# Optimization experiments

Hardware: AMD Instinct MI355X
Metric: run time of the kernel (lower is better)

The kernel has to match this reference:

```python
import jax, jax.numpy as jnp
import numpy as np

NUM_HEADS = 8
DIM = 64
DEPTH = DIM // NUM_HEADS  # 8
F = 64  # input feature dim


def setup_inputs() -> dict:
    key = jax.random.key(0)
    ks = jax.random.split(key, 5)
    x = jax.random.normal(ks[0], (4, 2048, F), dtype=jnp.float32)
    # per-head weights stacked: [H, F, depth]; initializer 'normal' ~ N(0, 0.05) in keras,
    # but scale does not change the math structure; use small normal.
    Wq = jax.random.normal(ks[1], (NUM_HEADS, F, DEPTH), dtype=jnp.float32) * 0.05
    Wk = jax.random.normal(ks[2], (NUM_HEADS, F, DEPTH), dtype=jnp.float32) * 0.05
    Wv = jax.random.normal(ks[3], (NUM_HEADS, F, DEPTH), dtype=jnp.float32) * 0.05
    Wo = jax.random.normal(ks[4], (NUM_HEADS * DEPTH, F), dtype=jnp.float32) * 0.05
    return {"x": x, "Wq": Wq, "Wk": Wk, "Wv": Wv, "Wo": Wo}


def reference(x, Wq, Wk, Wv, Wo):
    # x: [B, S, F]; Wq/Wk/Wv: [H, F, D]; Wo: [H*D, F]
    q = jnp.einsum("bsf,hfd->hbsd", x, Wq)
    k = jnp.einsum("bsf,hfd->hbsd", x, Wk)
    v = jnp.einsum("bsf,hfd->hbsd", x, Wv)
    scores = jnp.einsum("hbsd,hbtd->hbst", q, k) / jnp.sqrt(jnp.float32(DEPTH))
    weights = jax.nn.softmax(scores, axis=-1)  # [H, B, S, S]
    heads = jnp.einsum("hbst,hbtd->hbsd", weights, v)  # [H, B, S, D]
    # concat heads along last dim -> [B, S, H*D]
    B, S = x.shape[0], x.shape[1]
    concat = jnp.transpose(heads, (1, 2, 0, 3)).reshape(B, S, NUM_HEADS * DEPTH)
    out = concat @ Wo  # [B, S, F]
    # return_sequences=False -> sum over sequence axis
    return jnp.sum(out, axis=1), weights
```

## Files before the change

### kernel.cpp

```cpp
#include <hip/hip_runtime.h>
#include <cstdint>
#include <cstddef>

#define NH 8
#define NB 4
#define SS 2048
#define FF 64
#define DD 8
#define QKV_SZ (NH*NB*SS*DD)

typedef float f32x2 __attribute__((ext_vector_type(2)));

__device__ __forceinline__ f32x2 pkfma(f32x2 a, f32x2 b, f32x2 c) {
#if __has_builtin(__builtin_elementwise_fma)
  return __builtin_elementwise_fma(a, b, c);
#else
  f32x2 r; r.x = fmaf(a.x, b.x, c.x); r.y = fmaf(a.y, b.y, c.y); return r;
#endif
}

__device__ __forceinline__ float fastexp2(float x) {
#if __has_builtin(__builtin_amdgcn_exp2f)
  return __builtin_amdgcn_exp2f(x);
#else
  return exp2f(x);
#endif
}

__device__ __forceinline__ f32x2 lo2(float4 v) { f32x2 r; r.x = v.x; r.y = v.y; return r; }
__device__ __forceinline__ f32x2 hi2(float4 v) { f32x2 r; r.x = v.z; r.y = v.w; return r; }

__device__ __forceinline__ float wave_sum64(float x) {
#define DPP_STEP(ctrl, rm) { int t_ = __builtin_amdgcn_update_dpp(0, __float_as_int(x), (ctrl), (rm), 0xf, true); x += __int_as_float(t_); }
  DPP_STEP(0x111, 0xf)
  DPP_STEP(0x112, 0xf)
  DPP_STEP(0x114, 0xf)
  DPP_STEP(0x118, 0xf)
  DPP_STEP(0x142, 0xa)
  DPP_STEP(0x143, 0xc)
#undef DPP_STEP
  return x;
}

__global__ __launch_bounds__(256) void qkv_kernel(
    const float* __restrict__ x,
    const float* __restrict__ Wq, const float* __restrict__ Wk, const float* __restrict__ Wv,
    float* __restrict__ Qo, float* __restrict__ Ko, float* __restrict__ Vo) {
  __shared__ float xT[64][65];
  const int tid = threadIdx.x;
  const int row0 = blockIdx.x * 64;
  #pragma unroll
  for (int k = 0; k < 4; ++k) {
    int flat4 = tid + 256 * k;
    int r = flat4 >> 4, fq = flat4 & 15;
    float4 xv = reinterpret_cast<const float4*>(x)[(size_t)(row0 + r) * 16 + fq];
    xT[fq * 4 + 0][r] = xv.x; xT[fq * 4 + 1][r] = xv.y;
    xT[fq * 4 + 2][r] = xv.z; xT[fq * 4 + 3][r] = xv.w;
  }
  __syncthreads();
  const int r = tid & 63;
  const int wg = __builtin_amdgcn_readfirstlane((int)(blockIdx.y * 4 + (tid >> 6)));
  const float* Wmh[3];
  #pragma unroll
  for (int j = 0; j < 3; ++j) {
    int c = wg * 3 + j;
    int m = c >> 3, h = c & 7;
    const float* Wsel = (m == 0) ? Wq : ((m == 1) ? Wk : Wv);
    Wmh[j] = Wsel + (h << 9);
  }
  float acc[3][8];
  #pragma unroll
  for (int j = 0; j < 3; ++j)
    #pragma unroll
    for (int d = 0; d < 8; ++d) acc[j][d] = 0.f;
  for (int f = 0; f < 64; ++f) {
    float xv = xT[f][r];
    #pragma unroll
    for (int j = 0; j < 3; ++j) {
      const float4* wp = reinterpret_cast<const float4*>(Wmh[j] + f * 8);
      float4 wa = wp[0], wb = wp[1];
      acc[j][0] = fmaf(xv, wa.x, acc[j][0]); acc[j][1] = fmaf(xv, wa.y, acc[j][1]);
      acc[j][2] = fmaf(xv, wa.z, acc[j][2]); acc[j][3] = fmaf(xv, wa.w, acc[j][3]);
      acc[j][4] = fmaf(xv, wb.x, acc[j][4]); acc[j][5] = fmaf(xv, wb.y, acc[j][5]);
      acc[j][6] = fmaf(xv, wb.z, acc[j][6]); acc[j][7] = fmaf(xv, wb.w, acc[j][7]);
    }
  }
  const int row = row0 + r;
  const int b = row >> 11, s = row & 2047;
  const float qscale = 0.35355339059327373f * 1.4426950408889634f;
  #pragma unroll
  for (int j = 0; j < 3; ++j) {
    int c = wg * 3 + j;
    int m = c >> 3, h = c & 7;
    float sc = (m == 0) ? qscale : 1.f;
    float* dst = ((m == 0) ? Qo : ((m == 1) ? Ko : Vo)) + (((size_t)(h * NB + b) * SS) + s) * DD;
    float4 o0 = make_float4(acc[j][0] * sc, acc[j][1] * sc, acc[j][2] * sc, acc[j][3] * sc);
    float4 o1 = make_float4(acc[j][4] * sc, acc[j][5] * sc, acc[j][6] * sc, acc[j][7] * sc);
    reinterpret_cast<float4*>(dst)[0] = o0;
    reinterpret_cast<float4*>(dst)[1] = o1;
  }
}

__global__ __launch_bounds__(256, 4) void attn_kernel(
    const float* __restrict__ Qg, const float* __restrict__ Kg, const float* __restrict__ Vg,
    float* __restrict__ wOut, float* __restrict__ hsum2) {
  __shared__ float4 klds[4 * 512];
  __shared__ float4 qlds[128];
  __shared__ float psum[4][64];
  __shared__ float nls_s[64];
  __shared__ float hred[4][8];
  const int tid = threadIdx.x;
  const int lane = tid & 63;
  const int w = tid >> 6;
  const int bx = blockIdx.x;
  const int hb = bx >> 5;
  const int rt = bx & 31;
  const int r0 = rt * 64;
  const float* Kbase = Kg + (size_t)hb * SS * DD;
  const float* Vbase = Vg + (size_t)hb * SS * DD;
  const float4* K4 = reinterpret_cast<const float4*>(Kbase);
  const float4* Q4 = reinterpret_cast<const float4*>(Qg + (size_t)hb * SS * DD + (size_t)r0 * DD);
  float* wBase = wOut + (size_t)hb * SS * SS + (size_t)r0 * SS;

  if (tid < 128) qlds[tid] = Q4[tid];

  float4 qa = Q4[lane * 2], qb = Q4[lane * 2 + 1];
  f32x2 q01, q23, q45, q67;
  q01.x = qa.x; q01.y = qa.y; q23.x = qa.z; q23.y = qa.w;
  q45.x = qb.x; q45.y = qb.y; q67.x = qb.z; q67.y = qb.w;
  float rs0 = 0.f, rs1 = 0.f;
  float4* kw = klds + w * 512;
  for (int cc = 0; cc < 2; ++cc) {
    const int t0 = (w * 2 + cc) * 256;
    #pragma unroll
    for (int i = 0; i < 8; ++i) kw[lane + 64 * i] = K4[(size_t)t0 * 2 + lane + 64 * i];
    float4 a0 = kw[0], b0 = kw[1], a1 = kw[2], b1 = kw[3];
    float4 a2 = kw[4], b2 = kw[5], a3 = kw[6], b3 = kw[7];
    for (int tt = 0; tt < 256; tt += 4) {
      const int tn = (tt + 4 < 256) ? (tt + 4) : 0;
      float4 na0 = kw[2 * tn],     nb0 = kw[2 * tn + 1];
      float4 na1 = kw[2 * tn + 2], nb1 = kw[2 * tn + 3];
      float4 na2 = kw[2 * tn + 4], nb2 = kw[2 * tn + 5];
      float4 na3 = kw[2 * tn + 6], nb3 = kw[2 * tn + 7];
      f32x2 d0 = q01 * lo2(a0);
      d0 = pkfma(q23, hi2(a0), d0); d0 = pkfma(q45, lo2(b0), d0); d0 = pkfma(q67, hi2(b0), d0);
      f32x2 d1 = q01 * lo2(a1);
      d1 = pkfma(q23, hi2(a1), d1); d1 = pkfma(q45, lo2(b1), d1); d1 = pkfma(q67, hi2(b1), d1);
      f32x2 d2 = q01 * lo2(a2);
      d2 = pkfma(q23, hi2(a2), d2); d2 = pkfma(q45, lo2(b2), d2); d2 = pkfma(q67, hi2(b2), d2);
      f32x2 d3 = q01 * lo2(a3);
      d3 = pkfma(q23, hi2(a3), d3); d3 = pkfma(q45, lo2(b3), d3); d3 = pkfma(q67, hi2(b3), d3);
      rs0 += fastexp2(d0.x + d0.y) + fastexp2(d1.x + d1.y);
      rs1 += fastexp2(d2.x + d2.y) + fastexp2(d3.x + d3.y);
      a0 = na0; b0 = nb0; a1 = na1; b1 = nb1;
      a2 = na2; b2 = nb2; a3 = na3; b3 = nb3;
    }
  }
  psum[w][lane] = rs0 + rs1;
  __syncthreads();
  if (tid < 64)
    nls_s[tid] = -log2f(psum[0][tid] + psum[1][tid] + psum[2][tid] + psum[3][tid]);
  __syncthreads();

  float A[8] = {0.f, 0.f, 0.f, 0.f, 0.f, 0.f, 0.f, 0.f};
  for (int ci = 0; ci < 2; ++ci) {
    const int c = w * 2 + ci;
    const int tbase = c * 256;
    const int tl = tbase + 4 * lane;
    const float4* kp = reinterpret_cast<const float4*>(Kbase + (size_t)tl * DD);
    float4 k0a = kp[0], k0b = kp[1], k1a = kp[2], k1b = kp[3];
    float4 k2a = kp[4], k2b = kp[5], k3a = kp[6], k3b = kp[7];
    float4 qa2 = qlds[0], qb2 = qlds[1];
    float nl = nls_s[0];
    float cs0 = 0.f, cs1 = 0.f, cs2 = 0.f, cs3 = 0.f;
    for (int r = 0; r < 64; ++r) {
      const int rn = (r < 63) ? (r + 1) : 63;
      float4 na = qlds[rn * 2], nb = qlds[rn * 2 + 1];
      float nln = nls_s[rn];
      f32x2 p01, p23, p45, p67, seed;
      p01.x = qa2.x; p01.y = qa2.y; p23.x = qa2.z; p23.y = qa2.w;
      p45.x = qb2.x; p45.y = qb2.y; p67.x = qb2.z; p67.y = qb2.w;
      seed.x = nl; seed.y = 0.f;
      f32x2 d0 = pkfma(p01, lo2(k0a), seed);
      d0 = pkfma(p23, hi2(k0a), d0); d0 = pkfma(p45, lo2(k0b), d0); d0 = pkfma(p67, hi2(k0b), d0);
      f32x2 d1 = pkfma(p01, lo2(k1a), seed);
      d1 = pkfma(p23, hi2(k1a), d1); d1 = pkfma(p45, lo2(k1b), d1); d1 = pkfma(p67, hi2(k1b), d1);
      f32x2 d2 = pkfma(p01, lo2(k2a), seed);
      d2 = pkfma(p23, hi2(k2a), d2); d2 = pkfma(p45, lo2(k2b), d2); d2 = pkfma(p67, hi2(k2b), d2);
      f32x2 d3 = pkfma(p01, lo2(k3a), seed);
      d3 = pkfma(p23, hi2(k3a), d3); d3 = pkfma(p45, lo2(k3b), d3); d3 = pkfma(p67, hi2(k3b), d3);
      float p0 = fastexp2(d0.x + d0.y);
      float p1 = fastexp2(d1.x + d1.y);
      float p2 = fastexp2(d2.x + d2.y);
      float p3 = fastexp2(d3.x + d3.y);
      reinterpret_cast<float4*>(wBase + (size_t)r * SS + tl)[0] = make_float4(p0, p1, p2, p3);
      cs0 += p0; cs1 += p1; cs2 += p2; cs3 += p3;
      qa2 = na; qb2 = nb; nl = nln;
    }
    const float4* vp = reinterpret_cast<const float4*>(Vbase + (size_t)tl * DD);
    float4 v0a = vp[0], v0b = vp[1], v1a = vp[2], v1b = vp[3];
    float4 v2a = vp[4], v2b = vp[5], v3a = vp[6], v3b = vp[7];
    A[0] = fmaf(cs0, v0a.x, A[0]); A[0] = fmaf(cs1, v1a.x, A[0]);
    A[0] = fmaf(cs2, v2a.x, A[0]); A[0] = fmaf(cs3, v3a.x, A[0]);
    A[1] = fmaf(cs0, v0a.y, A[1]); A[1] = fmaf(cs1, v1a.y, A[1]);
    A[1] = fmaf(cs2, v2a.y, A[1]); A[1] = fmaf(cs3, v3a.y, A[1]);
    A[2] = fmaf(cs0, v0a.z, A[2]); A[2] = fmaf(cs1, v1a.z, A[2]);
    A[2] = fmaf(cs2, v2a.z, A[2]); A[2] = fmaf(cs3, v3a.z, A[2]);
    A[3] = fmaf(cs0, v0a.w, A[3]); A[3] = fmaf(cs1, v1a.w, A[3]);
    A[3] = fmaf(cs2, v2a.w, A[3]); A[3] = fmaf(cs3, v3a.w, A[3]);
    A[4] = fmaf(cs0, v0b.x, A[4]); A[4] = fmaf(cs1, v1b.x, A[4]);
    A[4] = fmaf(cs2, v2b.x, A[4]); A[4] = fmaf(cs3, v3b.x, A[4]);
    A[5] = fmaf(cs0, v0b.y, A[5]); A[5] = fmaf(cs1, v1b.y, A[5]);
    A[5] = fmaf(cs2, v2b.y, A[5]); A[5] = fmaf(cs3, v3b.y, A[5]);
    A[6] = fmaf(cs0, v0b.z, A[6]); A[6] = fmaf(cs1, v1b.z, A[6]);
    A[6] = fmaf(cs2, v2b.z, A[6]); A[6] = fmaf(cs3, v3b.z, A[6]);
    A[7] = fmaf(cs0, v0b.w, A[7]); A[7] = fmaf(cs1, v1b.w, A[7]);
    A[7] = fmaf(cs2, v2b.w, A[7]); A[7] = fmaf(cs3, v3b.w, A[7]);
  }

  #pragma unroll
  for (int d = 0; d < 8; ++d) {
    float t = wave_sum64(A[d]);
    if (lane == 63) hred[w][d] = t;
  }
  __syncthreads();
  if (tid < 8) {
    float t = hred[0][tid] + hred[1][tid] + hred[2][tid] + hred[3][tid];
    hsum2[(size_t)bx * 8 + tid] = t;
  }
}

__global__ __launch_bounds__(256) void out_kernel(
    const float* __restrict__ hsum2, const float* __restrict__ Wo,
    float* __restrict__ out) {
  __shared__ float ch[256];
  const int tid = threadIdx.x;
  {
    int hb = tid >> 3, d = tid & 7;
    float s = 0.f;
    for (int rtile = 0; rtile < 32; ++rtile) s += hsum2[(size_t)(hb * 32 + rtile) * 8 + d];
    ch[tid] = s;
  }
  __syncthreads();
  const int b = tid >> 6, f = tid & 63;
  float acc = 0.f;
  for (int h = 0; h < 8; ++h) {
    #pragma unroll
    for (int d = 0; d < 8; ++d) {
      acc = fmaf(ch[(h * 4 + b) * 8 + d], Wo[(h * 8 + d) * 64 + f], acc);
    }
  }
  out[b * 64 + f] = acc;
}

extern "C" void kernel_launch(void* const* d_in, const int* in_sizes, int n_in,
                              void* d_out, int out_size, void* d_ws, size_t ws_size,
                              hipStream_t stream) {
  const float* x  = (const float*)d_in[0];
  const float* Wq = (const float*)d_in[1];
  const float* Wk = (const float*)d_in[2];
  const float* Wv = (const float*)d_in[3];
  const float* Wo = (const float*)d_in[4];
  float* out = (float*)d_out;
  float* wts = out + 256;
  float* ws = (float*)d_ws;
  float* Q = ws;
  float* K = ws + QKV_SZ;
  float* V = ws + 2 * (size_t)QKV_SZ;
  float* hs = ws + 3 * (size_t)QKV_SZ;

  qkv_kernel<<<dim3(128, 2), 256, 0, stream>>>(x, Wq, Wk, Wv, Q, K, V);
  attn_kernel<<<1024, 256, 0, stream>>>(Q, K, V, wts, hs);
  out_kernel<<<1, 256, 0, stream>>>(hs, Wo, out);
}
```

Baseline: 575.6 us.

## Interleave row-sum and weight-write phases in 16-row chunks

The attention kernel now handles its 64 query rows in four chunks of 16. For each chunk it computes the softmax row sums (16 rows by 4 key groups per wave, reduced with shuffles) and then immediately writes that chunk's weights. The goal is to overlap the compute-heavy sum phase of one chunk with the store-heavy write phase of another across waves, rather than separating them into two large phases. The cost is K being reloaded into LDS four times per block instead of once, eight barriers instead of two, and extra shuffle reductions.

```diff
diff --git a/kernel.cpp b/kernel.cpp
--- a/kernel.cpp
+++ b/kernel.cpp
@@ -29,6 +29,11 @@
 
 __device__ __forceinline__ f32x2 lo2(float4 v) { f32x2 r; r.x = v.x; r.y = v.y; return r; }
 __device__ __forceinline__ f32x2 hi2(float4 v) { f32x2 r; r.x = v.z; r.y = v.w; return r; }
+
+__device__ __forceinline__ void barrier_lgkm() {
+  asm volatile("s_waitcnt lgkmcnt(0)" ::: "memory");
+  __builtin_amdgcn_s_barrier();
+}
 
 __device__ __forceinline__ float wave_sum64(float x) {
 #define DPP_STEP(ctrl, rm) { int t_ = __builtin_amdgcn_update_dpp(0, __float_as_int(x), (ctrl), (rm), 0xf, true); x += __int_as_float(t_); }
@@ -106,7 +111,7 @@
     float* __restrict__ wOut, float* __restrict__ hsum2) {
   __shared__ float4 klds[4 * 512];
   __shared__ float4 qlds[128];
-  __shared__ float psum[4][64];
+  __shared__ float psum[4][16];
   __shared__ float nls_s[64];
   __shared__ float hred[4][8];
   const int tid = threadIdx.x;
@@ -124,98 +129,112 @@
 
   if (tid < 128) qlds[tid] = Q4[tid];
 
-  float4 qa = Q4[lane * 2], qb = Q4[lane * 2 + 1];
-  f32x2 q01, q23, q45, q67;
-  q01.x = qa.x; q01.y = qa.y; q23.x = qa.z; q23.y = qa.w;
-  q45.x = qb.x; q45.y = qb.y; q67.x = qb.z; q67.y = qb.w;
-  float rs0 = 0.f, rs1 = 0.f;
+  const int rsub = lane & 15;
+  const int tgrp = lane >> 4;
   float4* kw = klds + w * 512;
-  for (int cc = 0; cc < 2; ++cc) {
-    const int t0 = (w * 2 + cc) * 256;
-    #pragma unroll
-    for (int i = 0; i < 8; ++i) kw[lane + 64 * i] = K4[(size_t)t0 * 2 + lane + 64 * i];
-    float4 a0 = kw[0], b0 = kw[1], a1 = kw[2], b1 = kw[3];
-    float4 a2 = kw[4], b2 = kw[5], a3 = kw[6], b3 = kw[7];
-    for (int tt = 0; tt < 256; tt += 4) {
-      const int tn = (tt + 4 < 256) ? (tt + 4) : 0;
-      float4 na0 = kw[2 * tn],     nb0 = kw[2 * tn + 1];
-      float4 na1 = kw[2 * tn + 2], nb1 = kw[2 * tn + 3];
-      float4 na2 = kw[2 * tn + 4], nb2 = kw[2 * tn + 5];
-      float4 na3 = kw[2 * tn + 6], nb3 = kw[2 * tn + 7];
-      f32x2 d0 = q01 * lo2(a0);
-      d0 = pkfma(q23, hi2(a0), d0); d0 = pkfma(q45, lo2(b0), d0); d0 = pkfma(q67, hi2(b0), d0);
-      f32x2 d1 = q01 * lo2(a1);
-      d1 = pkfma(q23, hi2(a1), d1); d1 = pkfma(q45, lo2(b1), d1); d1 = pkfma(q67, hi2(b1), d1);
-      f32x2 d2 = q01 * lo2(a2);
-      d2 = pkfma(q23, hi2(a2), d2); d2 = pkfma(q45, lo2(b2), d2); d2 = pkfma(q67, hi2(b2), d2);
-      f32x2 d3 = q01 * lo2(a3);
-      d3 = pkfma(q23, hi2(a3), d3); d3 = pkfma(q45, lo2(b3), d3); d3 = pkfma(q67, hi2(b3), d3);
-      rs0 += fastexp2(d0.x + d0.y) + fastexp2(d1.x + d1.y);
-      rs1 += fastexp2(d2.x + d2.y) + fastexp2(d3.x + d3.y);
-      a0 = na0; b0 = nb0; a1 = na1; b1 = nb1;
-      a2 = na2; b2 = nb2; a3 = na3; b3 = nb3;
-    }
-  }
-  psum[w][lane] = rs0 + rs1;
-  __syncthreads();
-  if (tid < 64)
-    nls_s[tid] = -log2f(psum[0][tid] + psum[1][tid] + psum[2][tid] + psum[3][tid]);
-  __syncthreads();
-
   float A[8] = {0.f, 0.f, 0.f, 0.f, 0.f, 0.f, 0.f, 0.f};
-  for (int ci = 0; ci < 2; ++ci) {
-    const int c = w * 2 + ci;
-    const int tbase = c * 256;
-    const int tl = tbase + 4 * lane;
-    const float4* kp = reinterpret_cast<const float4*>(Kbase + (size_t)tl * DD);
-    float4 k0a = kp[0], k0b = kp[1], k1a = kp[2], k1b = kp[3];
-    float4 k2a = kp[4], k2b = kp[5], k3a = kp[6], k3b = kp[7];
-    float4 qa2 = qlds[0], qb2 = qlds[1];
-    float nl = nls_s[0];
-    float cs0 = 0.f, cs1 = 0.f, cs2 = 0.f, cs3 = 0.f;
-    for (int r = 0; r < 64; ++r) {
-      const int rn = (r < 63) ? (r + 1) : 63;
-      float4 na = qlds[rn * 2], nb = qlds[rn * 2 + 1];
-      float nln = nls_s[rn];
-      f32x2 p01, p23, p45, p67, seed;
-      p01.x = qa2.x; p01.y = qa2.y; p23.x = qa2.z; p23.y = qa2.w;
-      p45.x = qb2.x; p45.y = qb2.y; p67.x = qb2.z; p67.y = qb2.w;
-      seed.x = nl; seed.y = 0.f;
-      f32x2 d0 = pkfma(p01, lo2(k0a), seed);
-      d0 = pkfma(p23, hi2(k0a), d0); d0 = pkfma(p45, lo2(k0b), d0); d0 = pkfma(p67, hi2(k0b), d0);
-      f32x2 d1 = pkfma(p01, lo2(k1a), seed);
-      d1 = pkfma(p23, hi2(k1a), d1); d1 = pkfma(p45, lo2(k1b), d1); d1 = pkfma(p67, hi2(k1b), d1);
-      f32x2 d2 = pkfma(p01, lo2(k2a), seed);
-      d2 = pkfma(p23, hi2(k2a), d2); d2 = pkfma(p45, lo2(k2b), d2); d2 = pkfma(p67, hi2(k2b), d2);
-      f32x2 d3 = pkfma(p01, lo2(k3a), seed);
-      d3 = pkfma(p23, hi2(k3a), d3); d3 = pkfma(p45, lo2(k3b), d3); d3 = pkfma(p67, hi2(k3b), d3);
-      float p0 = fastexp2(d0.x + d0.y);
-      float p1 = fastexp2(d1.x + d1.y);
-      float p2 = fastexp2(d2.x + d2.y);
-      float p3 = fastexp2(d3.x + d3.y);
-      reinterpret_cast<float4*>(wBase + (size_t)r * SS + tl)[0] = make_float4(p0, p1, p2, p3);
-      cs0 += p0; cs1 += p1; cs2 += p2; cs3 += p3;
-      qa2 = na; qb2 = nb; nl = nln;
-    }
-    const float4* vp = reinterpret_cast<const float4*>(Vbase + (size_t)tl * DD);
-    float4 v0a = vp[0], v0b = vp[1], v1a = vp[2], v1b = vp[3];
-    float4 v2a = vp[4], v2b = vp[5], v3a = vp[6], v3b = vp[7];
-    A[0] = fmaf(cs0, v0a.x, A[0]); A[0] = fmaf(cs1, v1a.x, A[0]);
-    A[0] = fmaf(cs2, v2a.x, A[0]); A[0] = fmaf(cs3, v3a.x, A[0]);
-    A[1] = fmaf(cs0, v0a.y, A[1]); A[1] = fmaf(cs1, v1a.y, A[1]);
-    A[1] = fmaf(cs2, v2a.y, A[1]); A[1] = fmaf(cs3, v3a.y, A[1]);
-    A[2] = fmaf(cs0, v0a.z, A[2]); A[2] = fmaf(cs1, v1a.z, A[2]);
-    A[2] = fmaf(cs2, v2a.z, A[2]); A[2] = fmaf(cs3, v3a.z, A[2]);
-    A[3] = fmaf(cs0, v0a.w, A[3]); A[3] = fmaf(cs1, v1a.w, A[3]);
-    A[3] = fmaf(cs2, v2a.w, A[3]); A[3] = fmaf(cs3, v3a.w, A[3]);
-    A[4] = fmaf(cs0, v0b.x, A[4]); A[4] = fmaf(cs1, v1b.x, A[4]);
-    A[4] = fmaf(cs2, v2b.x, A[4]); A[4] = fmaf(cs3, v3b.x, A[4]);
-    A[5] = fmaf(cs0, v0b.y, A[5]); A[5] = fmaf(cs1, v1b.y, A[5]);
-    A[5] = fmaf(cs2, v2b.y, A[5]); A[5] = fmaf(cs3, v3b.y, A[5]);
-    A[6] = fmaf(cs0, v0b.z, A[6]); A[6] = fmaf(cs1, v1b.z, A[6]);
-    A[6] = fmaf(cs2, v2b.z, A[6]); A[6] = fmaf(cs3, v3b.z, A[6]);
-    A[7] = fmaf(cs0, v0b.w, A[7]); A[7] = fmaf(cs1, v1b.w, A[7]);
-    A[7] = fmaf(cs2, v2b.w, A[7]); A[7] = fmaf(cs3, v3b.w, A[7]);
+
+  for (int c = 0; c < 4; ++c) {
+    const int qrow = c * 16 + rsub;
+    float4 qa = Q4[qrow * 2], qb = Q4[qrow * 2 + 1];
+    f32x2 q01, q23, q45, q67;
+    q01.x = qa.x; q01.y = qa.y; q23.x = qa.z; q23.y = qa.w;
+    q45.x = qb.x; q45.y = qb.y; q67.x = qb.z; q67.y = qb.w;
+    float rsA = 0.f, rsB = 0.f;
+    for (int cc = 0; cc < 2; ++cc) {
+      const int t0 = (w * 2 + cc) * 256;
+      #pragma unroll
+      for (int i = 0; i < 8; ++i) kw[lane + 64 * i] = K4[(size_t)t0 * 2 + lane + 64 * i];
+      float4 a0 = kw[2 * tgrp],        b0 = kw[2 * tgrp + 1];
+      float4 a1 = kw[2 * (tgrp + 4)],  b1 = kw[2 * (tgrp + 4) + 1];
+      float4 a2 = kw[2 * (tgrp + 8)],  b2 = kw[2 * (tgrp + 8) + 1];
+      float4 a3 = kw[2 * (tgrp + 12)], b3 = kw[2 * (tgrp + 12) + 1];
+      for (int j = 0; j < 64; j += 4) {
+        const int jn = (j + 4 < 64) ? (j + 4) : 0;
+        const int tb = tgrp + 4 * jn;
+        float4 na0 = kw[2 * tb],        nb0 = kw[2 * tb + 1];
+        float4 na1 = kw[2 * (tb + 4)],  nb1 = kw[2 * (tb + 4) + 1];
+        float4 na2 = kw[2 * (tb + 8)],  nb2 = kw[2 * (tb + 8) + 1];
+        float4 na3 = kw[2 * (tb + 12)], nb3 = kw[2 * (tb + 12) + 1];
+        f32x2 d0 = q01 * lo2(a0);
+        d0 = pkfma(q23, hi2(a0), d0); d0 = pkfma(q45, lo2(b0), d0); d0 = pkfma(q67, hi2(b0), d0);
+        f32x2 d1 = q01 * lo2(a1);
+        d1 = pkfma(q23, hi2(a1), d1); d1 = pkfma(q45, lo2(b1), d1); d1 = pkfma(q67, hi2(b1), d1);
+        f32x2 d2 = q01 * lo2(a2);
+        d2 = pkfma(q23, hi2(a2), d2); d2 = pkfma(q45, lo2(b2), d2); d2 = pkfma(q67, hi2(b2), d2);
+        f32x2 d3 = q01 * lo2(a3);
+        d3 = pkfma(q23, hi2(a3), d3); d3 = pkfma(q45, lo2(b3), d3); d3 = pkfma(q67, hi2(b3), d3);
+        rsA += fastexp2(d0.x + d0.y) + fastexp2(d1.x + d1.y);
+        rsB += fastexp2(d2.x + d2.y) + fastexp2(d3.x + d3.y);
+        a0 = na0; b0 = nb0; a1 = na1; b1 = nb1;
+        a2 = na2; b2 = nb2; a3 = na3; b3 = nb3;
+      }
+    }
+    float rs = rsA + rsB;
+    rs += __shfl_xor(rs, 16, 64);
+    rs += __shfl_xor(rs, 32, 64);
+    if (lane < 16) psum[w][lane] = rs;
+    barrier_lgkm();
+    if (tid < 16)
+      nls_s[c * 16 + tid] =
+          -log2f(psum[0][tid] + psum[1][tid] + psum[2][tid] + psum[3][tid]);
+    barrier_lgkm();
+
+    #pragma unroll
+    for (int ci = 0; ci < 2; ++ci) {
+      const int tbase = (w * 2 + ci) * 256;
+      const int tl = tbase + 4 * lane;
+      const float4* kp = reinterpret_cast<const float4*>(Kbase + (size_t)tl * DD);
+      float4 k0a = kp[0], k0b = kp[1], k1a = kp[2], k1b = kp[3];
+      float4 k2a = kp[4], k2b = kp[5], k3a = kp[6], k3b = kp[7];
+      float4 qa2 = qlds[(c * 16) * 2], qb2 = qlds[(c * 16) * 2 + 1];
+      float nl = nls_s[c * 16];
+      float cs0 = 0.f, cs1 = 0.f, cs2 = 0.f, cs3 = 0.f;
+      for (int rr = 0; rr < 16; ++rr) {
+        const int r = c * 16 + rr;
+        const int rn = (rr < 15) ? (r + 1) : r;
+        float4 na = qlds[rn * 2], nb = qlds[rn * 2 + 1];
+        float nln = nls_s[rn];
+        f32x2 p01, p23, p45, p67, seed;
+        p01.x = qa2.x; p01.y = qa2.y; p23.x = qa2.z; p23.y = qa2.w;
+        p45.x = qb2.x; p45.y = qb2.y; p67.x = qb2.z; p67.y = qb2.w;
+        seed.x = nl; seed.y = 0.f;
+        f32x2 d0 = pkfma(p01, lo2(k0a), seed);
+        d0 = pkfma(p23, hi2(k0a), d0); d0 = pkfma(p45, lo2(k0b), d0); d0 = pkfma(p67, hi2(k0b), d0);
+        f32x2 d1 = pkfma(p01, lo2(k1a), seed);
+        d1 = pkfma(p23, hi2(k1a), d1); d1 = pkfma(p45, lo2(k1b), d1); d1 = pkfma(p67, hi2(k1b), d1);
+        f32x2 d2 = pkfma(p01, lo2(k2a), seed);
+        d2 = pkfma(p23, hi2(k2a), d2); d2 = pkfma(p45, lo2(k2b), d2); d2 = pkfma(p67, hi2(k2b), d2);
+        f32x2 d3 = pkfma(p01, lo2(k3a), seed);
+        d3 = pkfma(p23, hi2(k3a), d3); d3 = pkfma(p45, lo2(k3b), d3); d3 = pkfma(p67, hi2(k3b), d3);
+        float p0 = fastexp2(d0.x + d0.y);
+        float p1 = fastexp2(d1.x + d1.y);
+        float p2 = fastexp2(d2.x + d2.y);
+        float p3 = fastexp2(d3.x + d3.y);
+        reinterpret_cast<float4*>(wBase + (size_t)r * SS + tl)[0] = make_float4(p0, p1, p2, p3);
+        cs0 += p0; cs1 += p1; cs2 += p2; cs3 += p3;
+        qa2 = na; qb2 = nb; nl = nln;
+      }
+      const float4* vp = reinterpret_cast<const float4*>(Vbase + (size_t)tl * DD);
+      float4 v0a = vp[0], v0b = vp[1], v1a = vp[2], v1b = vp[3];
+      float4 v2a = vp[4], v2b = vp[5], v3a = vp[6], v3b = vp[7];
+      A[0] = fmaf(cs0, v0a.x, A[0]); A[0] = fmaf(cs1, v1a.x, A[0]);
+      A[0] = fmaf(cs2, v2a.x, A[0]); A[0] = fmaf(cs3, v3a.x, A[0]);
+      A[1] = fmaf(cs0, v0a.y, A[1]); A[1] = fmaf(cs1, v1a.y, A[1]);
+      A[1] = fmaf(cs2, v2a.y, A[1]); A[1] = fmaf(cs3, v3a.y, A[1]);
+      A[2] = fmaf(cs0, v0a.z, A[2]); A[2] = fmaf(cs1, v1a.z, A[2]);
+      A[2] = fmaf(cs2, v2a.z, A[2]); A[2] = fmaf(cs3, v3a.z, A[2]);
+      A[3] = fmaf(cs0, v0a.w, A[3]); A[3] = fmaf(cs1, v1a.w, A[3]);
+      A[3] = fmaf(cs2, v2a.w, A[3]); A[3] = fmaf(cs3, v3a.w, A[3]);
+      A[4] = fmaf(cs0, v0b.x, A[4]); A[4] = fmaf(cs1, v1b.x, A[4]);
+      A[4] = fmaf(cs2, v2b.x, A[4]); A[4] = fmaf(cs3, v3b.x, A[4]);
+      A[5] = fmaf(cs0, v0b.y, A[5]); A[5] = fmaf(cs1, v1b.y, A[5]);
+      A[5] = fmaf(cs2, v2b.y, A[5]); A[5] = fmaf(cs3, v3b.y, A[5]);
+      A[6] = fmaf(cs0, v0b.z, A[6]); A[6] = fmaf(cs1, v1b.z, A[6]);
+      A[6] = fmaf(cs2, v2b.z, A[6]); A[6] = fmaf(cs3, v3b.z, A[6]);
+      A[7] = fmaf(cs0, v0b.w, A[7]); A[7] = fmaf(cs1, v1b.w, A[7]);
+      A[7] = fmaf(cs2, v2b.w, A[7]); A[7] = fmaf(cs3, v3b.w, A[7]);
+    }
   }
 
   #pragma unroll
```

Result: slower. 626.3 us (+8.8%).
